# Kernel optimization log

Measured on AMD Instinct MI355X. Metric: run time of the kernel, lower is better.

Reference implementation:

```python
import jax, jax.numpy as jnp
import numpy as np
from jax import lax

T, B, NIN, H, NOUT = 256, 64, 256, 2048, 256
DT, TAU, SIGMA = 20.0, 100.0, 0.05
DECAY = DT / TAU                      # alpha in the leaky-Euler update
NOISE_SCALE = SIGMA * float(np.sqrt(2.0 / DECAY))
MAX_INIT_STEPS = 100
ATOL = 0.1


def setup_inputs() -> dict:
    key = jax.random.key(0)
    k1, k2, k3, k4 = jax.random.split(key, 4)
    x = jax.random.normal(k1, (T, B, NIN), dtype=jnp.float32)
    W_ih = jax.random.normal(k2, (H, NIN), dtype=jnp.float32) / np.sqrt(NIN)
    # w_rec_init='diag': strong diagonal plus small random recurrent weights
    W_hh = 0.5 * jnp.eye(H, dtype=jnp.float32) + 0.1 * jax.random.normal(k3, (H, H), dtype=jnp.float32) / np.sqrt(H)
    b = jnp.zeros((H,), dtype=jnp.float32)
    W_out = jax.random.normal(k4, (NOUT, H), dtype=jnp.float32) / np.sqrt(H)
    return {"x": x, "W_ih": W_ih, "W_hh": W_hh, "b": b, "W_out": W_out}


def reference(x, W_ih, W_hh, b, W_out):
    base = jax.random.key(42)

    def cell(h, x_t, k):
        # leaky RNN step: h' = (1-a)h + a*relu(W_ih x + W_hh h + b + noise)
        pre = x_t @ W_ih.T + h @ W_hh.T + b
        pre = pre + NOISE_SCALE * jax.random.normal(k, pre.shape, dtype=pre.dtype)
        return (1.0 - DECAY) * h + DECAY * jax.nn.relu(pre)

    # ---- init_hidden_: up to 100 probe iterations of 2 steps on x[:2, 0:1] ----
    x_probe = x[:2, :1]                       # [2, 1, NIN], broadcasts vs h [B, H]
    h0_init = jnp.zeros((B, H), dtype=x.dtype)

    def init_body(carry, i):
        h0, stable, done = carry
        k = jax.random.fold_in(base, i)
        ka, kb = jax.random.split(k)
        h1 = cell(h0, x_probe[0], ka)
        h2 = cell(h1, x_probe[1], kb)
        close = jnp.max(jnp.abs(h2 - h0)) <= ATOL
        stable_new = jnp.where(done, stable, jnp.where(close, stable + 1, 0))
        trigger = (~done) & close & (stable_new >= 4)   # return pre-update h0
        done_new = done | trigger
        h0_new = jnp.where(done_new, h0, h2)
        return (h0_new, stable_new, done_new), None

    (h0, _, _), _ = lax.scan(init_body, (h0_init, jnp.int32(0), jnp.bool_(False)),
                             jnp.arange(MAX_INIT_STEPS))

    # ---- main unroll over T steps ----
    ks = jax.random.split(jax.random.fold_in(base, 1_000_000), T)

    def step(h, inp):
        x_t, k = inp
        h_new = cell(h, x_t, k)
        return h_new, h_new

    _, hidden = lax.scan(step, h0, (x, ks))   # [T, B, H]
    output = hidden @ W_out.T                 # [T, B, NOUT]
    return output, hidden
```

## Files before the change

kernel.cpp:

```cpp
#include <hip/hip_runtime.h>

typedef unsigned int u32;
typedef unsigned short u16;
typedef __bf16 bf16x8 __attribute__((ext_vector_type(8)));
typedef u16 us8 __attribute__((ext_vector_type(8)));
typedef u32 u32x2 __attribute__((ext_vector_type(2)));
typedef u32 u32x4 __attribute__((ext_vector_type(4)));
typedef float f32x4 __attribute__((ext_vector_type(4)));

#define T_N 256
#define B_N 64
#define NIN_N 256
#define H_N 2048
#define NOUT_N 256
#define BH (B_N * H_N)
#define OUT_SZ (T_N * B_N * NOUT_N)

struct U2 { u32 x, y; };

__device__ __forceinline__ u32 rotl32(u32 v, int r) { return (v << r) | (v >> (32 - r)); }

__device__ __forceinline__ U2 tf2x32(U2 k, U2 x) {
  u32 ks0 = k.x, ks1 = k.y, ks2 = k.x ^ k.y ^ 0x1BD11BDAu;
  x.x += ks0; x.y += ks1;
#define TFR(a) x.x += x.y; x.y = rotl32(x.y,(a)); x.y ^= x.x;
  TFR(13) TFR(15) TFR(26) TFR(6)
  x.x += ks1; x.y += ks2 + 1u;
  TFR(17) TFR(29) TFR(16) TFR(24)
  x.x += ks2; x.y += ks0 + 2u;
  TFR(13) TFR(15) TFR(26) TFR(6)
  x.x += ks0; x.y += ks1 + 3u;
  TFR(17) TFR(29) TFR(16) TFR(24)
  x.x += ks1; x.y += ks2 + 4u;
  TFR(13) TFR(15) TFR(26) TFR(6)
  x.x += ks2; x.y += ks0 + 5u;
#undef TFR
  return x;
}

__device__ __forceinline__ float jax_normal(u32 bits) {
  float f = __uint_as_float((bits >> 9) | 0x3f800000u) - 1.0f;
  const float lo = -0.99999994f;
  float u = fmaf(f, 2.0f, lo);
  u = fmaxf(u, lo);
  float w = -log1pf(-u * u);
  float p;
  if (w < 5.0f) {
    w = w - 2.5f;
    p =            2.81022636e-08f;
    p = fmaf(p, w, 3.43273939e-07f);
    p = fmaf(p, w, -3.5233877e-06f);
    p = fmaf(p, w, -4.39150654e-06f);
    p = fmaf(p, w, 0.00021858087f);
    p = fmaf(p, w, -0.00125372503f);
    p = fmaf(p, w, -0.00417768164f);
    p = fmaf(p, w, 0.246640727f);
    p = fmaf(p, w, 1.50140941f);
  } else {
    w = sqrtf(w) - 3.0f;
    p =            -0.000200214257f;
    p = fmaf(p, w, 0.000100950558f);
    p = fmaf(p, w, 0.00134934322f);
    p = fmaf(p, w, -0.00367342844f);
    p = fmaf(p, w, 0.00573950773f);
    p = fmaf(p, w, -0.0076224613f);
    p = fmaf(p, w, 0.00943887047f);
    p = fmaf(p, w, 1.00167406f);
    p = fmaf(p, w, 2.83297682f);
  }
  return 1.41421354f * (p * u);
}

__device__ __forceinline__ u16 f2bf(float f) {
  u32 x = __float_as_uint(f);
  u32 r = (x + 0x7FFFu + ((x >> 16) & 1u)) >> 16;
  return (u16)r;
}
__device__ __forceinline__ float bf2f(u16 b) { return __uint_as_float(((u32)b) << 16); }

__device__ __forceinline__ bf16x8 ld8(const u16* p) {
  us8 v = *reinterpret_cast<const us8*>(p);
  return __builtin_bit_cast(bf16x8, v);
}
__device__ __forceinline__ f32x4 mfma16(bf16x8 a, bf16x8 b, f32x4 c) {
  return __builtin_amdgcn_mfma_f32_16x16x32_bf16(a, b, c, 0, 0, 0);
}

__device__ __forceinline__ void st_agent_u16(u16* p, u16 v) {
  __hip_atomic_store(p, v, __ATOMIC_RELAXED, __HIP_MEMORY_SCOPE_AGENT);
}
__device__ __forceinline__ void st_agent_u32(u32* p, u32 v, int order) {
  if (order) __hip_atomic_store(p, v, __ATOMIC_RELEASE, __HIP_MEMORY_SCOPE_AGENT);
  else       __hip_atomic_store(p, v, __ATOMIC_RELAXED, __HIP_MEMORY_SCOPE_AGENT);
}
__device__ __forceinline__ u32 ld_agent_u32(const u32* p) {
  return __hip_atomic_load(p, __ATOMIC_RELAXED, __HIP_MEMORY_SCOPE_AGENT);
}

#define GLD16(AP, V) \
  asm volatile( \
    "global_load_dwordx4 %0, %16, off offset:-4096 sc0 sc1\n\t" \
    "global_load_dwordx4 %1, %16, off sc0 sc1\n\t" \
    "global_load_dwordx4 %2, %17, off offset:-4096 sc0 sc1\n\t" \
    "global_load_dwordx4 %3, %17, off sc0 sc1\n\t" \
    "global_load_dwordx4 %4, %18, off offset:-4096 sc0 sc1\n\t" \
    "global_load_dwordx4 %5, %18, off sc0 sc1\n\t" \
    "global_load_dwordx4 %6, %19, off offset:-4096 sc0 sc1\n\t" \
    "global_load_dwordx4 %7, %19, off sc0 sc1\n\t" \
    "global_load_dwordx4 %8, %20, off offset:-4096 sc0 sc1\n\t" \
    "global_load_dwordx4 %9, %20, off sc0 sc1\n\t" \
    "global_load_dwordx4 %10, %21, off offset:-4096 sc0 sc1\n\t" \
    "global_load_dwordx4 %11, %21, off sc0 sc1\n\t" \
    "global_load_dwordx4 %12, %22, off offset:-4096 sc0 sc1\n\t" \
    "global_load_dwordx4 %13, %22, off sc0 sc1\n\t" \
    "global_load_dwordx4 %14, %23, off offset:-4096 sc0 sc1\n\t" \
    "global_load_dwordx4 %15, %23, off sc0 sc1\n\t" \
    "s_waitcnt vmcnt(0)" \
    : "=&v"(V##0), "=&v"(V##1), "=&v"(V##2), "=&v"(V##3), \
      "=&v"(V##4), "=&v"(V##5), "=&v"(V##6), "=&v"(V##7), \
      "=&v"(V##8), "=&v"(V##9), "=&v"(V##10), "=&v"(V##11), \
      "=&v"(V##12), "=&v"(V##13), "=&v"(V##14), "=&v"(V##15) \
    : "v"(AP + 2048), "v"(AP + 3 * 2048), "v"(AP + 5 * 2048), "v"(AP + 7 * 2048), \
      "v"(AP + 9 * 2048), "v"(AP + 11 * 2048), "v"(AP + 13 * 2048), "v"(AP + 15 * 2048) \
    : "memory")

__global__ void __launch_bounds__(256) pack_b_kernel(const float* __restrict__ W,
    u16* __restrict__ hi, u16* __restrict__ lo, int K, int Cshift) {
  int tid = blockIdx.x * 256 + threadIdx.x;
  int lane = tid & 63;
  size_t tile = tid >> 6;
  int C = 1 << Cshift;
  int jt = (int)(tile >> Cshift), c = (int)(tile & (C - 1));
  int row = jt * 16 + (lane & 15);
  int k0 = c * 32 + (lane >> 4) * 8;
  const float* src = W + (size_t)row * K + k0;
  us8 vh, vl;
#pragma unroll
  for (int j = 0; j < 8; ++j) {
    float w = src[j];
    u16 hb = f2bf(w);
    vh[j] = hb;
    vl[j] = f2bf(w - bf2f(hb));
  }
  *reinterpret_cast<us8*>(hi + tile * 512 + lane * 8) = vh;
  *reinterpret_cast<us8*>(lo + tile * 512 + lane * 8) = vl;
}

__global__ void __launch_bounds__(256) pack_x_kernel(const float* __restrict__ x,
    u16* __restrict__ hi, u16* __restrict__ lo) {
  int tid = blockIdx.x * 256 + threadIdx.x;
  int t = tid >> 11;
  int r = tid & 2047;
  int lane = r & 63, piece = r >> 6;
  int c = piece >> 2, g = piece & 3;
  int row = g * 16 + (lane & 15);
  int k0 = c * 32 + (lane >> 4) * 8;
  const float* src = x + (size_t)t * (B_N * NIN_N) + (size_t)row * NIN_N + k0;
  us8 vh, vl;
#pragma unroll
  for (int j = 0; j < 8; ++j) {
    float w = src[j];
    u16 hb = f2bf(w);
    vh[j] = hb;
    vl[j] = f2bf(w - bf2f(hb));
  }
  size_t off = (size_t)t * 16384 + (size_t)piece * 512 + lane * 8;
  *reinterpret_cast<us8*>(hi + off) = vh;
  *reinterpret_cast<us8*>(lo + off) = vl;
}

__global__ void __launch_bounds__(256) probe_proj(const float* __restrict__ x,
    const float* __restrict__ Wih, const float* __restrict__ bias, float* __restrict__ xpj) {
  int g = blockIdx.x * 256 + threadIdx.x;
  int p = g >> 11, col = g & 2047;
  const float* xr = x + (size_t)p * (B_N * NIN_N);
  const float* wr = Wih + (size_t)col * NIN_N;
  float s = 0.f;
#pragma unroll 4
  for (int k = 0; k < NIN_N; ++k) s = fmaf(xr[k], wr[k], s);
  xpj[p * H_N + col] = s + bias[col];
}

__global__ void __launch_bounds__(256) xproj_gemm(const u16* __restrict__ xp_hi,
    const u16* __restrict__ xp_lo, const u16* __restrict__ wih_hi,
    const u16* __restrict__ wih_lo, const float* __restrict__ bias,
    float* __restrict__ xout) {
  int lane = threadIdx.x & 63, wvq = threadIdx.x >> 6;
  int t = blockIdx.x >> 7, jt16 = blockIdx.x & 127;
  const u16* ah = xp_hi + (size_t)t * 16384 + wvq * 512 + lane * 8;
  const u16* al = xp_lo + (size_t)t * 16384 + wvq * 512 + lane * 8;
  const u16* bh = wih_hi + (size_t)jt16 * 4096 + lane * 8;
  const u16* bl = wih_lo + (size_t)jt16 * 4096 + lane * 8;
  f32x4 z = {0.f, 0.f, 0.f, 0.f};
  f32x4 a0 = z, a1 = z, a2 = z;
#pragma unroll
  for (int c = 0; c < 8; ++c) {
    bf16x8 xh = ld8(ah + c * 2048), xl = ld8(al + c * 2048);
    bf16x8 wh = ld8(bh + c * 512),  wl = ld8(bl + c * 512);
    a0 = mfma16(xh, wh, a0);
    a1 = mfma16(xh, wl, a1);
    a2 = mfma16(xl, wh, a2);
  }
  f32x4 acc = (a0 + a1) + a2;
  int col = jt16 * 16 + (lane & 15);
  int q = lane >> 4;
  float bc = bias[col];
#pragma unroll
  for (int r = 0; r < 4; ++r) {
    int row = wvq * 16 + q * 4 + r;
    xout[(size_t)t * BH + (size_t)row * H_N + col] = acc[r] + bc;
  }
}

__global__ void setup_keys(U2* ka, U2* kb, U2* ks) {
  int i = threadIdx.x;
  U2 base{0u, 42u};
  if (i < 104) {
    U2 ki = tf2x32(base, U2{0u, (u32)i});
    ka[i] = tf2x32(ki, U2{0u, 0u});
    kb[i] = tf2x32(ki, U2{0u, 1u});
  }
  U2 km = tf2x32(base, U2{0u, 1000000u});
  ks[i] = tf2x32(km, U2{0u, (u32)i});
}

__global__ void __launch_bounds__(256) zero_bufs(u32* hx0w, u32* hx0lw, u32* bar) {
  int g = blockIdx.x * 256 + threadIdx.x;
  if (g < BH / 2) { hx0w[g] = 0u; hx0lw[g] = 0u; }
  if (g < 1024) bar[g] = 0u;
}

struct RnnParams {
  const u16 *whh_hi, *whh_lo;
  const float* xpj;
  float* hidden;
  u16 *hx0, *hx1, *hx2, *hxA, *hxB;
  u16 *hx0l, *hx1l, *hx2l;
  const U2 *ka, *kb, *ks;
  u32 *slots, *mslot;
};

__global__ void __launch_bounds__(512, 2) rnn_persistent(RnnParams P) {
  __shared__ f32x4 rbuf[512];
  __shared__ float red[16];

  const int lane = threadIdx.x & 63;
  const int wv = threadIdx.x >> 6;
  const int rg = wv >> 2;
  const int kh = wv & 3;
  const int blk = blockIdx.x;
  const int jt16 = blk & 127;
  const int rh = blk >> 7;
  const int bqg = rh * 2 + rg;
  const int q = lane >> 4;
  const int row = bqg * 16 + q * 4 + kh;
  const int col = jt16 * 16 + (lane & 15);
  const u32 idx = (u32)row * H_N + (u32)col;
  const u32 xoff = ((u32)((col >> 5) * 4 + (row >> 4)) * 64
                    + (u32)(((col >> 3) & 3) * 16 + (row & 15))) * 8 + (u32)(col & 7);

  bf16x8 Bh[16], Bl[16];
  {
    const u16* gbh = P.whh_hi + (size_t)jt16 * 32768 + kh * 8192 + lane * 8;
    const u16* gbl = P.whh_lo + (size_t)jt16 * 32768 + kh * 8192 + lane * 8;
#pragma unroll
    for (int c = 0; c < 16; ++c) {
      Bh[c] = ld8(gbh + c * 512);
      Bl[c] = ld8(gbl + c * 512);
    }
  }

  u32 ebar = 0;
  auto bar_cell = [&](bool agg) {
    ++ebar;
    asm volatile("s_waitcnt vmcnt(0)" ::: "memory");
    __syncthreads();
    if (wv == 0) {
      if (lane == 0) {
        if (agg) {
          float m = red[0];
#pragma unroll
          for (int w2 = 1; w2 < 8; ++w2) m = fmaxf(m, red[w2]);
          st_agent_u32(P.mslot + blk, __float_as_uint(m), 0);
        }
        st_agent_u32(P.slots + blk, ebar, 1);
      }
      if (agg) {
        const u32* ps = P.slots + lane * 4;
        for (;;) {
          u32x4 pr;
          asm volatile("global_load_dwordx4 %0, %1, off sc0 sc1\n\ts_waitcnt vmcnt(0)"
                       : "=&v"(pr) : "v"(ps) : "memory");
          u32 mn = pr.x < pr.y ? pr.x : pr.y;
          u32 mn2 = pr.z < pr.w ? pr.z : pr.w;
          mn = mn < mn2 ? mn : mn2;
          if (__all(mn >= ebar)) break;
          __builtin_amdgcn_s_sleep(1);
        }
        float m = fmaxf(fmaxf(__uint_as_float(ld_agent_u32(P.mslot + lane * 4 + 0)),
                              __uint_as_float(ld_agent_u32(P.mslot + lane * 4 + 1))),
                        fmaxf(__uint_as_float(ld_agent_u32(P.mslot + lane * 4 + 2)),
                              __uint_as_float(ld_agent_u32(P.mslot + lane * 4 + 3))));
#pragma unroll
        for (int o = 32; o >= 1; o >>= 1) m = fmaxf(m, __shfl_down(m, o));
        if (lane == 0) ((u32*)red)[8] = (m <= 0.1f) ? 1u : 0u;
      } else {
        const u32* ps = P.slots + rh * 128 + lane * 2;
        for (;;) {
          u32x2 pr;
          asm volatile("global_load_dwordx2 %0, %1, off sc0 sc1\n\ts_waitcnt vmcnt(0)"
                       : "=&v"(pr) : "v"(ps) : "memory");
          u32 mn = pr.x < pr.y ? pr.x : pr.y;
          if (__all(mn >= ebar)) break;
          __builtin_amdgcn_s_sleep(1);
        }
      }
    }
    __syncthreads();
  };

  auto reduce_av = [&](f32x4 acc) -> float {
    rbuf[wv * 64 + lane] = acc;
    __syncthreads();
    const float* rb = (const float*)(rbuf + rg * 256);
    return rb[lane * 4 + kh] + rb[256 + lane * 4 + kh]
         + rb[512 + lane * 4 + kh] + rb[768 + lane * 4 + kh];
  };

  auto gemm_hi = [&](const u16* hx_in) -> float {
    const u16* ap = hx_in + bqg * 512 + kh * 32768 + lane * 8;
    u32x4 A0, A1, A2, A3, A4, A5, A6, A7, A8, A9, A10, A11, A12, A13, A14, A15;
    GLD16(ap, A);
    f32x4 z = {0.f, 0.f, 0.f, 0.f};
    f32x4 a0 = z, a1 = z, a2 = z, a3 = z;
#define HSTEP(c, AV) { bf16x8 ah_ = __builtin_bit_cast(bf16x8, AV); \
    if ((c) & 1) { a2 = mfma16(ah_, Bh[c], a2); a3 = mfma16(ah_, Bl[c], a3); } \
    else { a0 = mfma16(ah_, Bh[c], a0); a1 = mfma16(ah_, Bl[c], a1); } }
    HSTEP(0, A0)  HSTEP(1, A1)  HSTEP(2, A2)  HSTEP(3, A3)
    HSTEP(4, A4)  HSTEP(5, A5)  HSTEP(6, A6)  HSTEP(7, A7)
    HSTEP(8, A8)  HSTEP(9, A9)  HSTEP(10, A10) HSTEP(11, A11)
    HSTEP(12, A12) HSTEP(13, A13) HSTEP(14, A14) HSTEP(15, A15)
#undef HSTEP
    return reduce_av((a0 + a1) + (a2 + a3));
  };

  auto gemm_hilo = [&](const u16* hx_in, const u16* hx_lo) -> float {
    const u16* aph = hx_in + bqg * 512 + kh * 32768 + lane * 8;
    const u16* apl = hx_lo + bqg * 512 + kh * 32768 + lane * 8;
    f32x4 z = {0.f, 0.f, 0.f, 0.f};
    f32x4 a0 = z, a1 = z, a2 = z, a3 = z, a4 = z, a5 = z;
    {
      u32x4 H0, H1, H2, H3, H4, H5, H6, H7, H8, H9, H10, H11, H12, H13, H14, H15;
      GLD16(aph, H);
#define ISTEP(c, AV) { bf16x8 ah_ = __builtin_bit_cast(bf16x8, AV); \
      if ((c) & 1) { a3 = mfma16(ah_, Bh[c], a3); a4 = mfma16(ah_, Bl[c], a4); } \
      else { a0 = mfma16(ah_, Bh[c], a0); a1 = mfma16(ah_, Bl[c], a1); } }
      ISTEP(0, H0)  ISTEP(1, H1)  ISTEP(2, H2)  ISTEP(3, H3)
      ISTEP(4, H4)  ISTEP(5, H5)  ISTEP(6, H6)  ISTEP(7, H7)
      ISTEP(8, H8)  ISTEP(9, H9)  ISTEP(10, H10) ISTEP(11, H11)
      ISTEP(12, H12) ISTEP(13, H13) ISTEP(14, H14) ISTEP(15, H15)
#undef ISTEP
    }
    {
      u32x4 L0, L1, L2, L3, L4, L5, L6, L7, L8, L9, L10, L11, L12, L13, L14, L15;
      GLD16(apl, L);
#define LSTEP(c, AV) { bf16x8 al_ = __builtin_bit_cast(bf16x8, AV); \
      if ((c) & 1) { a5 = mfma16(al_, Bh[c], a5); } \
      else { a2 = mfma16(al_, Bh[c], a2); } }
      LSTEP(0, L0)  LSTEP(1, L1)  LSTEP(2, L2)  LSTEP(3, L3)
      LSTEP(4, L4)  LSTEP(5, L5)  LSTEP(6, L6)  LSTEP(7, L7)
      LSTEP(8, L8)  LSTEP(9, L9)  LSTEP(10, L10) LSTEP(11, L11)
      LSTEP(12, L12) LSTEP(13, L13) LSTEP(14, L14) LSTEP(15, L15)
#undef LSTEP
    }
    return reduce_av(((a0 + a1) + (a2 + a3)) + (a4 + a5));
  };

  auto make_noise = [&](U2 key) -> float {
    U2 o = tf2x32(key, U2{0u, idx});
    return jax_normal(o.x ^ o.y);
  };

  const float NS = 0.15811388300841897f;
  const float xv0 = P.xpj[col];
  const float xv1 = P.xpj[H_N + col];

  u16* hxs[3]  = {P.hx0, P.hx1, P.hx2};
  u16* hxls[3] = {P.hx0l, P.hx1l, P.hx2l};
  int i0 = 0, i1 = 1, i2 = 2;
  float hp0 = 0.f;
  int stable = 0;
  float nzA = make_noise(P.ka[0]);
  float nzB = 0.f;

#pragma unroll 1
  for (int it = 0; it < 100; ++it) {
    float av = gemm_hilo(hxs[i0], hxls[i0]);
    float pre = av + xv0 + NS * nzA;
    float hp1 = 0.8f * hp0 + 0.2f * fmaxf(pre, 0.f);
    { u16 hb = f2bf(hp1);
      st_agent_u16(hxs[i1] + xoff, hb);
      st_agent_u16(hxls[i1] + xoff, f2bf(hp1 - bf2f(hb))); }
    nzB = make_noise(P.kb[it]);
    bar_cell(false);

    av = gemm_hilo(hxs[i1], hxls[i1]);
    pre = av + xv1 + NS * nzB;
    float hp2 = 0.8f * hp1 + 0.2f * fmaxf(pre, 0.f);
    { u16 hb = f2bf(hp2);
      st_agent_u16(hxs[i2] + xoff, hb);
      st_agent_u16(hxls[i2] + xoff, f2bf(hp2 - bf2f(hb))); }
    float lmax = fabsf(hp2 - hp0);
#pragma unroll
    for (int off = 32; off >= 1; off >>= 1)
      lmax = fmaxf(lmax, __shfl_down(lmax, off));
    if (lane == 0) red[wv] = lmax;
    nzA = make_noise(P.ka[it + 1]);
    bar_cell(true);

    bool close = (((u32*)red)[8] & 1u) != 0u;
    if (close) {
      if (++stable >= 4) break;
    } else stable = 0;
    int tmp = i0; i0 = i2; i2 = tmp;
    hp0 = hp2;
  }

  float nzS = make_noise(P.ks[0]);
  float xv = P.hidden[idx];
  float hp = hp0;
#pragma unroll 1
  for (int t = 0; t < T_N; ++t) {
    const u16* hin = (t == 0) ? hxs[i0] : (((t - 1) & 1) ? P.hxB : P.hxA);
    float av = gemm_hi(hin);
    float pre = av + xv + NS * nzS;
    float hn = 0.8f * hp + 0.2f * fmaxf(pre, 0.f);
    hp = hn;
    st_agent_u16(((t & 1) ? P.hxB : P.hxA) + xoff, f2bf(hn));
    if (t != T_N - 1) {
      nzS = make_noise(P.ks[t + 1]);
      bar_cell(false);
      P.hidden[(size_t)t * BH + idx] = hn;
      xv = P.hidden[(size_t)(t + 1) * BH + idx];
    } else {
      P.hidden[(size_t)t * BH + idx] = hn;
    }
  }
}

__global__ void __launch_bounds__(256) out_gemm(const float* __restrict__ hidden,
    const u16* __restrict__ wo_hi, const u16* __restrict__ wo_lo, float* __restrict__ out) {
  int lane = threadIdx.x & 63, wv = threadIdx.x >> 6;
  int mb = blockIdx.x * 64 + wv * 16;
  int arow = mb + (lane & 15);
  int q = lane >> 4;
  f32x4 acc[16];
#pragma unroll
  for (int n = 0; n < 16; ++n) acc[n] = {0.f, 0.f, 0.f, 0.f};
  const float* ap = hidden + (size_t)arow * H_N + q * 8;
#pragma unroll 2
  for (int c = 0; c < 64; ++c) {
    const float4* a4 = reinterpret_cast<const float4*>(ap + c * 32);
    float4 f0 = a4[0], f1 = a4[1];
    us8 av;
    av[0] = f2bf(f0.x); av[1] = f2bf(f0.y); av[2] = f2bf(f0.z); av[3] = f2bf(f0.w);
    av[4] = f2bf(f1.x); av[5] = f2bf(f1.y); av[6] = f2bf(f1.z); av[7] = f2bf(f1.w);
    bf16x8 a = __builtin_bit_cast(bf16x8, av);
#pragma unroll
    for (int n = 0; n < 16; ++n) {
      bf16x8 bh = ld8(wo_hi + ((size_t)(n * 64 + c) * 64 + lane) * 8);
      bf16x8 bl = ld8(wo_lo + ((size_t)(n * 64 + c) * 64 + lane) * 8);
      acc[n] = mfma16(a, bh, acc[n]);
      acc[n] = mfma16(a, bl, acc[n]);
    }
  }
#pragma unroll
  for (int n = 0; n < 16; ++n)
#pragma unroll
    for (int r = 0; r < 4; ++r)
      out[(size_t)(mb + q * 4 + r) * NOUT_N + n * 16 + (lane & 15)] = acc[n][r];
}

extern "C" void kernel_launch(void* const* d_in, const int* in_sizes, int n_in,
                              void* d_out, int out_size, void* d_ws, size_t ws_size,
                              hipStream_t stream) {
  const float* x = (const float*)d_in[0];
  const float* W_ih = (const float*)d_in[1];
  const float* W_hh = (const float*)d_in[2];
  const float* bias = (const float*)d_in[3];
  const float* W_out = (const float*)d_in[4];
  float* out = (float*)d_out;

  char* ws = (char*)d_ws;
  size_t off = 0;
  auto alloc = [&](size_t bytes) -> void* {
    void* p = ws + off;
    off += (bytes + 255) & ~(size_t)255;
    return p;
  };
  u16* whh_hi = (u16*)alloc(8388608);
  u16* whh_lo = (u16*)alloc(8388608);
  u16* wih_hi = (u16*)alloc(1048576);
  u16* wih_lo = (u16*)alloc(1048576);
  u16* wout_hi = (u16*)alloc(1048576);
  u16* wout_lo = (u16*)alloc(1048576);
  u16* xp_hi = (u16*)alloc(8388608);
  u16* xp_lo = (u16*)alloc(8388608);
  float* xpj = (float*)alloc(16384);
  u16* hx0 = (u16*)alloc(262144);
  u16* hx1 = (u16*)alloc(262144);
  u16* hx2 = (u16*)alloc(262144);
  u16* hxA = (u16*)alloc(262144);
  u16* hxB = (u16*)alloc(262144);
  u16* hx0l = (u16*)alloc(262144);
  u16* hx1l = (u16*)alloc(262144);
  u16* hx2l = (u16*)alloc(262144);
  U2* ka = (U2*)alloc(832);
  U2* kb = (U2*)alloc(832);
  U2* ks = (U2*)alloc(2048);
  u32* bar = (u32*)alloc(4096);

  float* hidden = out + OUT_SZ;

  hipLaunchKernelGGL(pack_b_kernel, dim3(2048), dim3(256), 0, stream, W_hh, whh_hi, whh_lo, 2048, 6);
  hipLaunchKernelGGL(pack_b_kernel, dim3(256), dim3(256), 0, stream, W_ih, wih_hi, wih_lo, 256, 3);
  hipLaunchKernelGGL(pack_b_kernel, dim3(256), dim3(256), 0, stream, W_out, wout_hi, wout_lo, 2048, 6);
  hipLaunchKernelGGL(pack_x_kernel, dim3(2048), dim3(256), 0, stream, x, xp_hi, xp_lo);
  hipLaunchKernelGGL(probe_proj, dim3(16), dim3(256), 0, stream, x, W_ih, bias, xpj);
  hipLaunchKernelGGL(setup_keys, dim3(1), dim3(256), 0, stream, ka, kb, ks);
  hipLaunchKernelGGL(zero_bufs, dim3(256), dim3(256), 0, stream, (u32*)hx0, (u32*)hx0l, bar);
  hipLaunchKernelGGL(xproj_gemm, dim3(32768), dim3(256), 0, stream, xp_hi, xp_lo, wih_hi, wih_lo, bias, hidden);

  RnnParams P;
  P.whh_hi = whh_hi; P.whh_lo = whh_lo;
  P.xpj = xpj;
  P.hidden = hidden;
  P.hx0 = hx0; P.hx1 = hx1; P.hx2 = hx2; P.hxA = hxA; P.hxB = hxB;
  P.hx0l = hx0l; P.hx1l = hx1l; P.hx2l = hx2l;
  P.ka = ka; P.kb = kb; P.ks = ks;
  P.slots = bar; P.mslot = bar + 256;

  void* kargs[] = {(void*)&P};
  hipLaunchCooperativeKernel((const void*)rnn_persistent, dim3(256), dim3(512), kargs, 0, stream);

  hipLaunchKernelGGL(out_gemm, dim3(256), dim3(256), 0, stream, hidden, wout_hi, wout_lo, out);
}
```

Before: 5.388 ms.

## Use a fresh hidden-state buffer per timestep to allow cached loads

```diff
diff --git a/kernel.cpp b/kernel.cpp
--- a/kernel.cpp
+++ b/kernel.cpp
@@ -234,13 +234,14 @@
   const u16 *whh_hi, *whh_lo;
   const float* xpj;
   float* hidden;
-  u16 *hx0, *hx1, *hx2, *hxA, *hxB;
+  u16 *hx0, *hx1, *hx2;
   u16 *hx0l, *hx1l, *hx2l;
+  u16 *hxstep;
   const U2 *ka, *kb, *ks;
   u32 *slots, *mslot;
 };
 
-__global__ void __launch_bounds__(512, 2) rnn_persistent(RnnParams P) {
+__global__ void __launch_bounds__(512, 1) rnn_persistent(RnnParams P) {
   __shared__ f32x4 rbuf[512];
   __shared__ float red[16];
 
@@ -327,20 +328,18 @@
          + rb[512 + lane * 4 + kh] + rb[768 + lane * 4 + kh];
   };
 
-  auto gemm_hi = [&](const u16* hx_in) -> float {
+  auto gemm_hi_cached = [&](const u16* hx_in) -> float {
     const u16* ap = hx_in + bqg * 512 + kh * 32768 + lane * 8;
-    u32x4 A0, A1, A2, A3, A4, A5, A6, A7, A8, A9, A10, A11, A12, A13, A14, A15;
-    GLD16(ap, A);
+    bf16x8 A[16];
+#pragma unroll
+    for (int c = 0; c < 16; ++c) A[c] = ld8(ap + c * 2048);
     f32x4 z = {0.f, 0.f, 0.f, 0.f};
     f32x4 a0 = z, a1 = z, a2 = z, a3 = z;
-#define HSTEP(c, AV) { bf16x8 ah_ = __builtin_bit_cast(bf16x8, AV); \
-    if ((c) & 1) { a2 = mfma16(ah_, Bh[c], a2); a3 = mfma16(ah_, Bl[c], a3); } \
-    else { a0 = mfma16(ah_, Bh[c], a0); a1 = mfma16(ah_, Bl[c], a1); } }
-    HSTEP(0, A0)  HSTEP(1, A1)  HSTEP(2, A2)  HSTEP(3, A3)
-    HSTEP(4, A4)  HSTEP(5, A5)  HSTEP(6, A6)  HSTEP(7, A7)
-    HSTEP(8, A8)  HSTEP(9, A9)  HSTEP(10, A10) HSTEP(11, A11)
-    HSTEP(12, A12) HSTEP(13, A13) HSTEP(14, A14) HSTEP(15, A15)
-#undef HSTEP
+#pragma unroll
+    for (int c = 0; c < 16; ++c) {
+      if (c & 1) { a2 = mfma16(A[c], Bh[c], a2); a3 = mfma16(A[c], Bl[c], a3); }
+      else       { a0 = mfma16(A[c], Bh[c], a0); a1 = mfma16(A[c], Bl[c], a1); }
+    }
     return reduce_av((a0 + a1) + (a2 + a3));
   };
 
@@ -426,17 +425,18 @@
     hp0 = hp2;
   }
 
+  st_agent_u16(P.hxstep + xoff, f2bf(hp0));
   float nzS = make_noise(P.ks[0]);
   float xv = P.hidden[idx];
+  bar_cell(false);
   float hp = hp0;
 #pragma unroll 1
   for (int t = 0; t < T_N; ++t) {
-    const u16* hin = (t == 0) ? hxs[i0] : (((t - 1) & 1) ? P.hxB : P.hxA);
-    float av = gemm_hi(hin);
+    float av = gemm_hi_cached(P.hxstep + (size_t)t * BH);
     float pre = av + xv + NS * nzS;
     float hn = 0.8f * hp + 0.2f * fmaxf(pre, 0.f);
     hp = hn;
-    st_agent_u16(((t & 1) ? P.hxB : P.hxA) + xoff, f2bf(hn));
+    st_agent_u16(P.hxstep + (size_t)(t + 1) * BH + xoff, f2bf(hn));
     if (t != T_N - 1) {
       nzS = make_noise(P.ks[t + 1]);
       bar_cell(false);
@@ -510,8 +510,6 @@
   u16* hx0 = (u16*)alloc(262144);
   u16* hx1 = (u16*)alloc(262144);
   u16* hx2 = (u16*)alloc(262144);
-  u16* hxA = (u16*)alloc(262144);
-  u16* hxB = (u16*)alloc(262144);
   u16* hx0l = (u16*)alloc(262144);
   u16* hx1l = (u16*)alloc(262144);
   u16* hx2l = (u16*)alloc(262144);
@@ -519,6 +517,7 @@
   U2* kb = (U2*)alloc(832);
   U2* ks = (U2*)alloc(2048);
   u32* bar = (u32*)alloc(4096);
+  u16* hxstep = (u16*)alloc((size_t)257 * 262144);
 
   float* hidden = out + OUT_SZ;
 
@@ -535,8 +534,9 @@
   P.whh_hi = whh_hi; P.whh_lo = whh_lo;
   P.xpj = xpj;
   P.hidden = hidden;
-  P.hx0 = hx0; P.hx1 = hx1; P.hx2 = hx2; P.hxA = hxA; P.hxB = hxB;
+  P.hx0 = hx0; P.hx1 = hx1; P.hx2 = hx2;
   P.hx0l = hx0l; P.hx1l = hx1l; P.hx2l = hx2l;
+  P.hxstep = hxstep;
   P.ka = ka; P.kb = kb; P.ks = ks;
   P.slots = bar; P.mslot = bar + 256;
 
```

After: 5.532 ms. 1.03x slower.
